# Optimization experiments

Measured on AMD Instinct MI355X. Metric: run time of the kernel, lower is better.

## Reference

```python
import jax, jax.numpy as jnp
import numpy as np

MD = 4  # max_displacement
NEG_SLOPE = 0.1  # LeakyReLU slope


def setup_inputs() -> dict:
    key = jax.random.key(0)
    k1, k2 = jax.random.split(key)
    B, H, W, C = 8, 128, 192, 128
    x1 = jax.random.normal(k1, (B, H, W, C), dtype=jnp.float32)
    warped = jax.random.normal(k2, (B, H, W, C), dtype=jnp.float32)
    return {"x1": x1, "warped": warped}


def reference(x1, warped):
    # cost[b,h,w,k] = mean_c x1[b,h,w,c] * warped[b,h+sh,w+sw,c]  (zero-padded)
    # k enumerates (sh, sw) in row-major order over [-MD, MD] x [-MD, MD].
    md = MD
    B, H, W, C = x1.shape
    wp = jnp.pad(warped, ((0, 0), (md, md), (md, md), (0, 0)))
    cv = []
    for sh in range(-md, md + 1):
        for sw in range(-md, md + 1):
            shifted = jax.lax.dynamic_slice(wp, (0, md + sh, md + sw, 0), (B, H, W, C))
            cv.append(jnp.mean(x1 * shifted, axis=3))
    cv = jnp.stack(cv, axis=3)  # [B, H, W, (2*md+1)**2]
    return jnp.where(cv >= 0, cv, NEG_SLOPE * cv)
```

## Files before the change

kernel.cpp:

```cpp
#include <hip/hip_runtime.h>


namespace {
constexpr int Bb = 8, Hh = 128, Ww = 192, Cn = 128;
constexpr int MDc = 4;
constexpr int TH = 8, TWT = 16;
constexpr int NTHR = 512;
constexpr int RH = 16;
constexpr int RPX = 24;
constexpr int KC = 32;
constexpr int NCH = Cn / KC;
constexpr int KQB = RPX * 16 + 16;
constexpr int ROWB = 4 * KQB;
constexpr int BUFB = RH * ROWB;
constexpr int RUNS = RH * RPX * 4;
constexpr int NIT = RUNS / NTHR;
constexpr float NEG = 0.1f;
}

typedef __fp16 h2v   __attribute__((ext_vector_type(2)));
typedef __fp16 f16x8 __attribute__((ext_vector_type(8)));
typedef float  f32x4 __attribute__((ext_vector_type(4)));

__device__ __forceinline__ unsigned pkh2(float a, float b) {
    h2v h = __builtin_amdgcn_cvt_pkrtz(a, b);
    return __builtin_bit_cast(unsigned, h);
}

__device__ __forceinline__ void barrier_lgkm() {
    asm volatile("s_waitcnt lgkmcnt(0)\n\ts_barrier" ::: "memory");
}

__global__ __launch_bounds__(NTHR, 4)
void costvol_mfma(const float* __restrict__ x1,
                  const float* __restrict__ wp,
                  float* __restrict__ out)
{
    __shared__ __align__(16) unsigned char smem[2 * BUFB];

    const int tid  = threadIdx.x;
    const int wv   = tid >> 6;
    const int lane = tid & 63;
    const int nI   = lane & 15;
    const int kq   = lane >> 4;

    const int id = blockIdx.x;
    const int wg = (id & 7) * 192 + (id >> 3);
    const int bx = wg % 12;
    const int t2 = wg / 12;
    const int by = t2 & 15;
    const int bz = t2 >> 4;

    const int w0 = bx * TWT;
    const int h0 = by * TH;
    const int b  = bz;

    int g_off[NIT]; int l_off[NIT]; bool g_ok[NIT];
#pragma unroll
    for (int it = 0; it < NIT; ++it) {
        int s   = tid + it * NTHR;
        int skq = s & 3;
        int t   = s >> 2;
        int px  = t % RPX;
        int row = t / RPX;
        int hw  = h0 - MDc + row;
        int ww  = w0 - MDc + px;
        bool ok = (unsigned)hw < (unsigned)Hh && (unsigned)ww < (unsigned)Ww;
        g_ok[it]  = ok;
        g_off[it] = ((b * Hh + (ok ? hw : 0)) * Ww + (ok ? ww : 0)) * Cn + skq * 8;
        l_off[it] = row * ROWB + skq * KQB + ((px ^ (skq << 1)) * 16);
    }

    uint4 gpA[NIT], gpB[NIT];
    auto LOADA = [&](int ch) {
#pragma unroll
        for (int it = 0; it < NIT; ++it) {
            if (g_ok[it]) {
                const float* p = wp + g_off[it] + ch * KC;
                float4 u = *reinterpret_cast<const float4*>(p);
                float4 v = *reinterpret_cast<const float4*>(p + 4);
                gpA[it] = make_uint4(pkh2(u.x, u.y), pkh2(u.z, u.w),
                                     pkh2(v.x, v.y), pkh2(v.z, v.w));
            } else {
                gpA[it] = make_uint4(0u, 0u, 0u, 0u);
            }
        }
    };
    auto LOADB = [&](int ch) {
#pragma unroll
        for (int it = 0; it < NIT; ++it) {
            if (g_ok[it]) {
                const float* p = wp + g_off[it] + ch * KC;
                float4 u = *reinterpret_cast<const float4*>(p);
                float4 v = *reinterpret_cast<const float4*>(p + 4);
                gpB[it] = make_uint4(pkh2(u.x, u.y), pkh2(u.z, u.w),
                                     pkh2(v.x, v.y), pkh2(v.z, v.w));
            } else {
                gpB[it] = make_uint4(0u, 0u, 0u, 0u);
            }
        }
    };
    auto WRITEA = [&](int buf) {
#pragma unroll
        for (int it = 0; it < NIT; ++it)
            *reinterpret_cast<uint4*>(smem + buf * BUFB + l_off[it]) = gpA[it];
    };
    auto WRITEB = [&](int buf) {
#pragma unroll
        for (int it = 0; it < NIT; ++it)
            *reinterpret_cast<uint4*>(smem + buf * BUFB + l_off[it]) = gpB[it];
    };

    LOADA(0);
    LOADB(1);

    const float* xp = x1 + ((size_t)((b * Hh + h0 + wv) * Ww) + w0 + nI) * Cn + kq * 8;
    float4 ar_u = *reinterpret_cast<const float4*>(xp);
    float4 ar_v = *reinterpret_cast<const float4*>(xp + 4);

    f32x4 ac0[9], ac1[9];
#pragma unroll
    for (int s = 0; s < 9; ++s) {
        f32x4 z = {0.f, 0.f, 0.f, 0.f};
        ac0[s] = z; ac1[s] = z;
    }

    const int ro0 = kq * KQB + ((nI ^ (kq << 1)) * 16);

    WRITEA(0);
    LOADA(2);

    int cur = 0;
#pragma unroll
    for (int ch = 0; ch < NCH; ++ch) {
        barrier_lgkm();
        if (ch == 0) { WRITEB(1); LOADB(3); }
        if (ch == 1) { WRITEA(0); }
        if (ch == 2) { WRITEB(1); }
        uint4 afr = make_uint4(pkh2(ar_u.x, ar_u.y), pkh2(ar_u.z, ar_u.w),
                               pkh2(ar_v.x, ar_v.y), pkh2(ar_v.z, ar_v.w));
        if (ch + 1 < NCH) {
            ar_u = *reinterpret_cast<const float4*>(xp + (ch + 1) * KC);
            ar_v = *reinterpret_cast<const float4*>(xp + (ch + 1) * KC + 4);
        }
        f16x8 av = __builtin_bit_cast(f16x8, afr);
        const unsigned char* base = smem + cur * BUFB;
#pragma unroll
        for (int sh = 0; sh < 9; ++sh) {
            const unsigned char* rp = base + (wv + sh) * ROWB;
            uint4 b0 = *reinterpret_cast<const uint4*>(rp + ro0);
            uint4 b1 = *reinterpret_cast<const uint4*>(rp + ro0 + 128);
            ac0[sh] = __builtin_amdgcn_mfma_f32_16x16x32_f16(
                av, __builtin_bit_cast(f16x8, b0), ac0[sh], 0, 0, 0);
            ac1[sh] = __builtin_amdgcn_mfma_f32_16x16x32_f16(
                av, __builtin_bit_cast(f16x8, b1), ac1[sh], 0, 0, 0);
        }
        cur ^= 1;
    }

    const float sc = 1.0f / (float)Cn;
    const size_t rowbase = ((size_t)((b * Hh + h0 + wv) * Ww) + w0) * 81;
#pragma unroll
    for (int rg = 0; rg < 4; ++rg) {
        int m = kq * 4 + rg;
        int d = nI - m;
        bool t0 = (d >= 0 && d <= 8);
        bool t1 = (d >= -8 && d <= 0 && nI >= 8);
        size_t mb = rowbase + (size_t)m * 81;
#pragma unroll
        for (int sh = 0; sh < 9; ++sh) {
            if (t0) {
                float v = ac0[sh][rg] * sc;
                out[mb + sh * 9 + d] = fmaxf(v, NEG * v);
            }
            if (t1) {
                float v = ac1[sh][rg] * sc;
                out[mb + sh * 9 + d + 8] = fmaxf(v, NEG * v);
            }
        }
    }
}

extern "C" void kernel_launch(void* const* d_in, const int* in_sizes, int n_in,
                              void* d_out, int out_size, void* d_ws, size_t ws_size,
                              hipStream_t stream) {
    const float* x1 = (const float*)d_in[0];
    const float* wp = (const float*)d_in[1];
    float* out = (float*)d_out;
    dim3 grid(12 * 16 * 8, 1, 1);
    costvol_mfma<<<grid, NTHR, 0, stream>>>(x1, wp, out);
}
```

Before: 55.25 us.

## Process two tiles per workgroup and prefetch the second tile during the first

The grid is halved so each workgroup computes two output tiles in sequence. Global loads for the second tile are issued while the first tile's last chunks are still being computed, so the next tile's loads overlap the current tile's MFMA work and launch/prologue cost is amortized. The LDS row padding is also removed, shrinking shared memory per block but possibly adding bank conflicts that the XOR swizzle may not fully hide. Register pressure rises from the extra offset state and the longer unrolled body.

Result: slower. 108.2 us (+95.8%).

```diff
diff --git a/kernel.cpp b/kernel.cpp
--- a/kernel.cpp
+++ b/kernel.cpp
@@ -10,7 +10,7 @@
 constexpr int RPX = 24;
 constexpr int KC = 32;
 constexpr int NCH = Cn / KC;
-constexpr int KQB = RPX * 16 + 16;
+constexpr int KQB = RPX * 16;
 constexpr int ROWB = 4 * KQB;
 constexpr int BUFB = RH * ROWB;
 constexpr int RUNS = RH * RPX * 4;
@@ -44,32 +44,39 @@
     const int nI   = lane & 15;
     const int kq   = lane >> 4;
 
-    const int id = blockIdx.x;
-    const int wg = (id & 7) * 192 + (id >> 3);
-    const int bx = wg % 12;
-    const int t2 = wg / 12;
-    const int by = t2 & 15;
-    const int bz = t2 >> 4;
-
-    const int w0 = bx * TWT;
-    const int h0 = by * TH;
-    const int b  = bz;
-
-    int g_off[NIT]; int l_off[NIT]; bool g_ok[NIT];
+    const int kb   = blockIdx.x;
+    const int xcd  = kb & 7;
+    const int base = kb >> 3;
+    const int wg0  = xcd * 192 + base;
+
+    int w0, h0, b0_;
+    {
+        int bx = wg0 % 12, t2 = wg0 / 12;
+        w0 = bx * TWT; h0 = (t2 & 15) * TH; b0_ = t2 >> 4;
+    }
+    int w1 = 0, h1 = 0, b1_ = 0;
+
+    int l_off[NIT];
 #pragma unroll
     for (int it = 0; it < NIT; ++it) {
-        int s   = tid + it * NTHR;
-        int skq = s & 3;
-        int t   = s >> 2;
-        int px  = t % RPX;
-        int row = t / RPX;
-        int hw  = h0 - MDc + row;
-        int ww  = w0 - MDc + px;
-        bool ok = (unsigned)hw < (unsigned)Hh && (unsigned)ww < (unsigned)Ww;
-        g_ok[it]  = ok;
-        g_off[it] = ((b * Hh + (ok ? hw : 0)) * Ww + (ok ? ww : 0)) * Cn + skq * 8;
+        int s = tid + it * NTHR, skq = s & 3, t = s >> 2;
+        int px = t % RPX, row = t / RPX;
         l_off[it] = row * ROWB + skq * KQB + ((px ^ (skq << 1)) * 16);
     }
+
+    int g_off[NIT]; bool g_ok[NIT];
+    auto OFFS = [&](int tw0, int th0, int tb) {
+#pragma unroll
+        for (int it = 0; it < NIT; ++it) {
+            int s = tid + it * NTHR, skq = s & 3, t = s >> 2;
+            int px = t % RPX, row = t / RPX;
+            int hw = th0 - MDc + row, ww = tw0 - MDc + px;
+            bool ok = (unsigned)hw < (unsigned)Hh && (unsigned)ww < (unsigned)Ww;
+            g_ok[it]  = ok;
+            g_off[it] = ((tb * Hh + (ok ? hw : 0)) * Ww + (ok ? ww : 0)) * Cn + skq * 8;
+        }
+    };
+    OFFS(w0, h0, b0_);
 
     uint4 gpA[NIT], gpB[NIT];
     auto LOADA = [&](int ch) {
@@ -114,7 +121,8 @@
     LOADA(0);
     LOADB(1);
 
-    const float* xp = x1 + ((size_t)((b * Hh + h0 + wv) * Ww) + w0 + nI) * Cn + kq * 8;
+    const float* xp  = x1 + ((size_t)((b0_ * Hh + h0 + wv) * Ww) + w0 + nI) * Cn + kq * 8;
+    const float* xp2 = xp;
     float4 ar_u = *reinterpret_cast<const float4*>(xp);
     float4 ar_v = *reinterpret_cast<const float4*>(xp + 4);
 
@@ -130,53 +138,87 @@
     WRITEA(0);
     LOADA(2);
 
-    int cur = 0;
-#pragma unroll
-    for (int ch = 0; ch < NCH; ++ch) {
-        barrier_lgkm();
-        if (ch == 0) { WRITEB(1); LOADB(3); }
-        if (ch == 1) { WRITEA(0); }
-        if (ch == 2) { WRITEB(1); }
-        uint4 afr = make_uint4(pkh2(ar_u.x, ar_u.y), pkh2(ar_u.z, ar_u.w),
-                               pkh2(ar_v.x, ar_v.y), pkh2(ar_v.z, ar_v.w));
-        if (ch + 1 < NCH) {
-            ar_u = *reinterpret_cast<const float4*>(xp + (ch + 1) * KC);
-            ar_v = *reinterpret_cast<const float4*>(xp + (ch + 1) * KC + 4);
-        }
-        f16x8 av = __builtin_bit_cast(f16x8, afr);
-        const unsigned char* base = smem + cur * BUFB;
-#pragma unroll
-        for (int sh = 0; sh < 9; ++sh) {
-            const unsigned char* rp = base + (wv + sh) * ROWB;
-            uint4 b0 = *reinterpret_cast<const uint4*>(rp + ro0);
-            uint4 b1 = *reinterpret_cast<const uint4*>(rp + ro0 + 128);
-            ac0[sh] = __builtin_amdgcn_mfma_f32_16x16x32_f16(
-                av, __builtin_bit_cast(f16x8, b0), ac0[sh], 0, 0, 0);
-            ac1[sh] = __builtin_amdgcn_mfma_f32_16x16x32_f16(
-                av, __builtin_bit_cast(f16x8, b1), ac1[sh], 0, 0, 0);
-        }
-        cur ^= 1;
-    }
-
     const float sc = 1.0f / (float)Cn;
-    const size_t rowbase = ((size_t)((b * Hh + h0 + wv) * Ww) + w0) * 81;
-#pragma unroll
-    for (int rg = 0; rg < 4; ++rg) {
-        int m = kq * 4 + rg;
-        int d = nI - m;
-        bool t0 = (d >= 0 && d <= 8);
-        bool t1 = (d >= -8 && d <= 0 && nI >= 8);
-        size_t mb = rowbase + (size_t)m * 81;
-#pragma unroll
-        for (int sh = 0; sh < 9; ++sh) {
-            if (t0) {
-                float v = ac0[sh][rg] * sc;
-                out[mb + sh * 9 + d] = fmaxf(v, NEG * v);
-            }
-            if (t1) {
-                float v = ac1[sh][rg] * sc;
-                out[mb + sh * 9 + d + 8] = fmaxf(v, NEG * v);
-            }
+
+#pragma unroll
+    for (int pass = 0; pass < 2; ++pass) {
+#pragma unroll
+        for (int ch = 0; ch < NCH; ++ch) {
+            barrier_lgkm();
+            if (pass == 0) {
+                if (ch == 0) { WRITEB(1); LOADB(3); }
+                if (ch == 1) {
+                    WRITEA(0);
+                    int wg1 = wg0 + 96;
+                    int bx = wg1 % 12, t2 = wg1 / 12;
+                    w1 = bx * TWT; h1 = (t2 & 15) * TH; b1_ = t2 >> 4;
+                    OFFS(w1, h1, b1_);
+                    xp2 = x1 + ((size_t)((b1_ * Hh + h1 + wv) * Ww) + w1 + nI) * Cn + kq * 8;
+                    LOADA(0);
+                }
+                if (ch == 2) { WRITEB(1); LOADB(1); }
+                if (ch == 3) { WRITEA(0); LOADA(2); }
+            } else {
+                if (ch == 0) { WRITEB(1); LOADB(3); }
+                if (ch == 1) { WRITEA(0); }
+                if (ch == 2) { WRITEB(1); }
+            }
+            uint4 afr = make_uint4(pkh2(ar_u.x, ar_u.y), pkh2(ar_u.z, ar_u.w),
+                                   pkh2(ar_v.x, ar_v.y), pkh2(ar_v.z, ar_v.w));
+            if (pass == 0) {
+                if (ch < 3) {
+                    ar_u = *reinterpret_cast<const float4*>(xp + (ch + 1) * KC);
+                    ar_v = *reinterpret_cast<const float4*>(xp + (ch + 1) * KC + 4);
+                } else {
+                    ar_u = *reinterpret_cast<const float4*>(xp2);
+                    ar_v = *reinterpret_cast<const float4*>(xp2 + 4);
+                }
+            } else if (ch < 3) {
+                ar_u = *reinterpret_cast<const float4*>(xp2 + (ch + 1) * KC);
+                ar_v = *reinterpret_cast<const float4*>(xp2 + (ch + 1) * KC + 4);
+            }
+            f16x8 av = __builtin_bit_cast(f16x8, afr);
+            const unsigned char* bse = smem + (ch & 1) * BUFB;
+#pragma unroll
+            for (int sh = 0; sh < 9; ++sh) {
+                const unsigned char* rp = bse + (wv + sh) * ROWB;
+                uint4 b0 = *reinterpret_cast<const uint4*>(rp + ro0);
+                uint4 b1 = *reinterpret_cast<const uint4*>(rp + ro0 + 128);
+                ac0[sh] = __builtin_amdgcn_mfma_f32_16x16x32_f16(
+                    av, __builtin_bit_cast(f16x8, b0), ac0[sh], 0, 0, 0);
+                ac1[sh] = __builtin_amdgcn_mfma_f32_16x16x32_f16(
+                    av, __builtin_bit_cast(f16x8, b1), ac1[sh], 0, 0, 0);
+            }
+        }
+
+        const size_t rowbase = ((size_t)((b0_ * Hh + h0 + wv) * Ww) + w0) * 81;
+#pragma unroll
+        for (int rg = 0; rg < 4; ++rg) {
+            int m = kq * 4 + rg;
+            int d = nI - m;
+            bool t0 = (d >= 0 && d <= 8);
+            bool t1 = (d >= -8 && d <= 0 && nI >= 8);
+            size_t mb = rowbase + (size_t)m * 81;
+#pragma unroll
+            for (int sh = 0; sh < 9; ++sh) {
+                if (t0) {
+                    float v = ac0[sh][rg] * sc;
+                    out[mb + sh * 9 + d] = fmaxf(v, NEG * v);
+                }
+                if (t1) {
+                    float v = ac1[sh][rg] * sc;
+                    out[mb + sh * 9 + d + 8] = fmaxf(v, NEG * v);
+                }
+            }
+        }
+
+        if (pass == 0) {
+#pragma unroll
+            for (int s = 0; s < 9; ++s) {
+                f32x4 z = {0.f, 0.f, 0.f, 0.f};
+                ac0[s] = z; ac1[s] = z;
+            }
+            w0 = w1; h0 = h1; b0_ = b1_;
         }
     }
 }
@@ -187,6 +229,6 @@
     const float* x1 = (const float*)d_in[0];
     const float* wp = (const float*)d_in[1];
     float* out = (float*)d_out;
-    dim3 grid(12 * 16 * 8, 1, 1);
+    dim3 grid(768, 1, 1);
     costvol_mfma<<<grid, NTHR, 0, stream>>>(x1, wp, out);
 }
```
